# Kernel tuning notes

Hardware: AMD Instinct MI355X
Metric: run time of the kernel (lower is better)

## Reference

```python
import jax, jax.numpy as jnp
import numpy as np

H = 64
N_G, E_G = 30000, 60000
N_LG, E_LG = 60000, 60000


def setup_inputs() -> dict:
    key = jax.random.key(0)
    ks = jax.random.split(key, 30)
    rn = lambda k, s, sc=0.05: jax.random.normal(k, s, jnp.float32) * sc
    return {
        "gx": jax.random.normal(ks[0], (N_G, 20), jnp.float32),
        "g_edge_index": jax.random.randint(ks[1], (2, E_G), 0, N_G, jnp.int32),
        "g_edge_attr": jax.random.uniform(ks[2], (E_G, 4), dtype=jnp.float32),
        "lgx": jax.random.normal(ks[3], (N_LG, 5), jnp.float32),
        "lg_edge_index": jax.random.randint(ks[4], (2, E_LG), 0, N_LG, jnp.int32),
        "lg_edge_attr": jax.random.uniform(ks[5], (E_LG, 1), dtype=jnp.float32),
        "adduct": jax.random.normal(ks[6], (3,), jnp.float32),
        "lin0_w": rn(ks[7], (20, H)), "lin0_b": rn(ks[8], (H,)),
        "g_nn_w1": rn(ks[9], (4, H)), "g_nn_b1": rn(ks[10], (H,)),
        "g_nn_w2": rn(ks[11], (H, H * H), 0.01), "g_nn_b2": rn(ks[12], (H * H,), 0.01),
        "g_root": rn(ks[13], (H, H)), "g_bias": rn(ks[14], (H,)),
        "lin0_lg_w": rn(ks[15], (5, H)), "lin0_lg_b": rn(ks[16], (H,)),
        "lg_nn_w1": rn(ks[17], (1, H)), "lg_nn_b1": rn(ks[18], (H,)),
        "lg_nn_w2": rn(ks[19], (H, H * H), 0.01), "lg_nn_b2": rn(ks[20], (H * H,), 0.01),
        "lg_root": rn(ks[21], (H, H)), "lg_bias": rn(ks[22], (H,)),
        "bott_w": rn(ks[23], (H + H + 3, 384)), "bott_b": rn(ks[24], (384,)),
        "lin1_w": rn(ks[25], (384, 384)), "lin1_b": rn(ks[26], (384,)),
        "lin2_w": rn(ks[27], (384, 1)), "lin2_b": rn(ks[28], (1,)),
    }


def _ecc_branch(x_in, edge_index, edge_attr, w1, b1, w2, b2, root, bias, n_iters, num_nodes):
    """N iterations of NNConv(aggr='mean') + ReLU, then sum pool over nodes."""
    src, tgt = edge_index[0], edge_index[1]  # source->target flow (PyG default)
    # edge MLP -> per-edge [in, out] weight (edge_attr is loop-invariant, compute once)
    W = (jax.nn.relu(edge_attr @ w1 + b1) @ w2 + b2).reshape(-1, H, H)  # [E, H, H]
    cnt = jnp.maximum(
        jax.ops.segment_sum(jnp.ones((tgt.shape[0],), x_in.dtype), tgt, num_segments=num_nodes),
        1.0,
    )
    x = x_in
    for _ in range(n_iters):
        msg = jnp.einsum('ei,eio->eo', x[src], W)  # gather + batched matvec
        agg = jax.ops.segment_sum(msg, tgt, num_segments=num_nodes) / cnt[:, None]  # scatter-mean
        x = jax.nn.relu(x @ root + agg + bias)  # root transform + bias (NNConv defaults)
    return x.sum(axis=0)  # sum pooling -> [H]


def reference(gx, g_edge_index, g_edge_attr, lgx, lg_edge_index, lg_edge_attr, adduct,
              lin0_w, lin0_b, g_nn_w1, g_nn_b1, g_nn_w2, g_nn_b2, g_root, g_bias,
              lin0_lg_w, lin0_lg_b, lg_nn_w1, lg_nn_b1, lg_nn_w2, lg_nn_b2, lg_root, lg_bias,
              bott_w, bott_b, lin1_w, lin1_b, lin2_w, lin2_b):
    out_g = _ecc_branch(jax.nn.relu(gx @ lin0_w + lin0_b), g_edge_index, g_edge_attr,
                        g_nn_w1, g_nn_b1, g_nn_w2, g_nn_b2, g_root, g_bias, 3, N_G)
    out_lg = _ecc_branch(jax.nn.relu(lgx @ lin0_lg_w + lin0_lg_b), lg_edge_index, lg_edge_attr,
                         lg_nn_w1, lg_nn_b1, lg_nn_w2, lg_nn_b2, lg_root, lg_bias, 3, N_LG)
    out = jnp.concatenate([out_g, out_lg, adduct], axis=-1)  # [131]
    out = jax.nn.relu(out @ bott_w + bott_b)
    for _ in range(6):
        out = jax.nn.relu(out @ lin1_w + lin1_b)
    return out @ lin2_w + lin2_b  # [1]
```

## Files before the change

kernel.cpp:

```cpp
#include <hip/hip_runtime.h>

typedef unsigned short u16;
using short8_t  = __attribute__((ext_vector_type(8)))  short;
using float16_t = __attribute__((ext_vector_type(16))) float;
using float2v   = __attribute__((ext_vector_type(2)))  float;

#define NKT 260
#define DEG_CAP 32

__device__ __forceinline__ float bf2f(u16 b) { return __uint_as_float(((unsigned)b) << 16); }
__device__ __forceinline__ u16 f2bf(float f) {
  unsigned u = __float_as_uint(f);
  return (u16)((u + 0x7fffu + ((u >> 16) & 1u)) >> 16);
}

union U8 { short8_t s; uint4 v; unsigned u[4]; };

__device__ __forceinline__ short8_t scale8p(const float2v* xf2, float2v h2) {
  U8 out;
  #pragma unroll
  for (int p = 0; p < 4; ++p) {
    float2v r = xf2[p] * h2;
    out.u[p] = __builtin_amdgcn_perm(__float_as_uint(r[1]), __float_as_uint(r[0]), 0x07060302);
  }
  return out.s;
}

template<int IN>
__device__ __forceinline__ void affine_body(
    const float* __restrict__ Xin, const float* __restrict__ W, const float* __restrict__ Bv,
    u16* __restrict__ Xout, int N, int gid)
{
  int n = gid >> 6, o = gid & 63;
  if (n >= N) return;
  float acc = Bv[o];
  #pragma unroll
  for (int i = 0; i < IN; ++i)
    acc = fmaf(Xin[n * IN + i], W[i * 64 + o], acc);
  Xout[gid] = f2bf(fmaxf(acc, 0.f));
}

__global__ __launch_bounds__(256) void affine_all_kernel(
    const float* __restrict__ gx, const float* __restrict__ l0w, const float* __restrict__ l0b, u16* __restrict__ xg,
    const float* __restrict__ lgx, const float* __restrict__ llw, const float* __restrict__ llb, u16* __restrict__ xl,
    const float* __restrict__ gea, const float* __restrict__ gw1, const float* __restrict__ gb1, u16* __restrict__ hg,
    const float* __restrict__ lea, const float* __restrict__ lw1, const float* __restrict__ lb1, u16* __restrict__ hl,
    int B0, int B1, int B2, int NG, int NLG, int EG, int ELG)
{
  int b = blockIdx.x, t = threadIdx.x;
  if (b < B0)       affine_body<20>(gx, l0w, l0b, xg, NG, b * 256 + t);
  else if (b < B1)  affine_body<5>(lgx, llw, llb, xl, NLG, (b - B0) * 256 + t);
  else if (b < B2)  affine_body<4>(gea, gw1, gb1, hg, EG, (b - B1) * 256 + t);
  else              affine_body<1>(lea, lw1, lb1, hl, ELG, (b - B2) * 256 + t);
}

__device__ __forceinline__ void bpack_body(
    const float* __restrict__ w2, const float* __restrict__ b2, u16* __restrict__ Bp, int gid)
{
  if (gid >= NKT * 128) return;
  int lane = gid & 63;
  int nt = (gid >> 6) & 1;
  int kt = gid >> 7;
  int o = nt * 32 + (lane & 31);
  int kbase = kt * 16 + (lane >> 5) * 8;
  u16 vals[8];
  #pragma unroll
  for (int j = 0; j < 8; ++j) {
    int k = kbase + j;
    vals[j] = f2bf((k < 4096) ? w2[(k >> 6) * 4096 + (k & 63) * 64 + o]
                              : b2[(k - 4096) * 64 + o]);
  }
  uint4 pack;
  pack.x = (unsigned)vals[0] | ((unsigned)vals[1] << 16);
  pack.y = (unsigned)vals[2] | ((unsigned)vals[3] << 16);
  pack.z = (unsigned)vals[4] | ((unsigned)vals[5] << 16);
  pack.w = (unsigned)vals[6] | ((unsigned)vals[7] << 16);
  *(uint4*)(Bp + (size_t)gid * 8) = pack;
}

__device__ __forceinline__ void rootpack_body(const float* __restrict__ root, u16* __restrict__ Rp, int gid)
{
  if (gid >= 512) return;
  int lane = gid & 63;
  int nt = (gid >> 6) & 1;
  int kt = gid >> 7;
  int o = nt * 32 + (lane & 31);
  int kbase = kt * 16 + (lane >> 5) * 8;
  u16 vals[8];
  #pragma unroll
  for (int j = 0; j < 8; ++j) vals[j] = f2bf(root[(kbase + j) * 64 + o]);
  uint4 pack;
  pack.x = (unsigned)vals[0] | ((unsigned)vals[1] << 16);
  pack.y = (unsigned)vals[2] | ((unsigned)vals[3] << 16);
  pack.z = (unsigned)vals[4] | ((unsigned)vals[5] << 16);
  pack.w = (unsigned)vals[6] | ((unsigned)vals[7] << 16);
  *(uint4*)(Rp + (size_t)gid * 8) = pack;
}

__global__ __launch_bounds__(256) void pack_all_kernel(
    const float* __restrict__ gw2, const float* __restrict__ gb2, u16* __restrict__ bpg,
    const float* __restrict__ lw2, const float* __restrict__ lb2, u16* __restrict__ bpl,
    const float* __restrict__ groot, u16* __restrict__ rpg,
    const float* __restrict__ lroot, u16* __restrict__ rpl)
{
  int b = blockIdx.x, t = threadIdx.x;
  if (b < 130)       bpack_body(gw2, gb2, bpg, b * 256 + t);
  else if (b < 260)  bpack_body(lw2, lb2, bpl, (b - 130) * 256 + t);
  else if (b < 262)  rootpack_body(groot, rpg, (b - 260) * 256 + t);
  else               rootpack_body(lroot, rpl, (b - 262) * 256 + t);
}

__device__ __forceinline__ void hist_body(
    const int* __restrict__ eidx, int* __restrict__ cnt, int* __restrict__ elist, int E, int e)
{
  if (e < E) {
    int tg = eidx[E + e];
    int pos = atomicAdd(cnt + tg, 1);
    if (pos < DEG_CAP) elist[(size_t)tg * DEG_CAP + pos] = e;
  }
}

__global__ __launch_bounds__(256) void hist_kernel(
    const int* __restrict__ eig, int* __restrict__ cg, int* __restrict__ elg, int Eg, int nbg,
    const int* __restrict__ eil, int* __restrict__ cl, int* __restrict__ ell, int El)
{
  int b = blockIdx.x, t = threadIdx.x;
  if (b < nbg) hist_body(eig, cg, elg, Eg, b * 256 + t);
  else         hist_body(eil, cl, ell, El, (b - nbg) * 256 + t);
}

__global__ __launch_bounds__(256, 4) void msg_gemm_kernel(
    const u16* __restrict__ Xg, const u16* __restrict__ Hg, const u16* __restrict__ Bg,
    const int* __restrict__ eig, u16* __restrict__ Mg, int Eg, int nbg,
    const u16* __restrict__ Xl, const u16* __restrict__ Hl, const u16* __restrict__ Bl,
    const int* __restrict__ eil, u16* __restrict__ Ml, int El)
{
  __shared__ __align__(16) u16 sB[4][4096];

  const int b = blockIdx.x;
  const u16 *X, *Hh, *Bp; const int* eidx; u16* msg; int E, e0;
  if (b < nbg) { X = Xg; Hh = Hg; Bp = Bg; eidx = eig; msg = Mg; E = Eg; e0 = b * 128; }
  else         { X = Xl; Hh = Hl; Bp = Bl; eidx = eil; msg = Ml; E = El; e0 = (b - nbg) * 128; }

  const int t = threadIdx.x;
  const int lane = t & 63;
  const int wid = t >> 6;
  const int ml = lane & 31;
  const int q  = lane >> 5;

  #pragma unroll
  for (int c0 = 0; c0 < 3; ++c0) {
    const u16* src = Bp + (size_t)c0 * 4096 + (size_t)wid * 1024 + (size_t)lane * 8;
    u16* dst = &sB[c0][wid * 1024];
    __builtin_amdgcn_global_load_lds((const __attribute__((address_space(1))) void*)src,
                                     (__attribute__((address_space(3))) void*)dst, 16, 0, 0);
    __builtin_amdgcn_global_load_lds((const __attribute__((address_space(1))) void*)(src + 512),
                                     (__attribute__((address_space(3))) void*)(dst + 512), 16, 0, 0);
  }

  const int ea  = e0 + wid * 32 + ml;
  const int eac = ea < E ? ea : E - 1;
  const int sa  = eidx[eac];

  float2v xf2[4][4];
  {
    const u16* xp = X + (size_t)sa * 64 + q * 8;
    #pragma unroll
    for (int s = 0; s < 4; ++s) {
      U8 va;
      va.v = *(const uint4*)(xp + s * 16);
      #pragma unroll
      for (int p = 0; p < 4; ++p) {
        float2v r;
        r[0] = __uint_as_float(va.u[p] << 16);
        r[1] = __uint_as_float(va.u[p] & 0xffff0000u);
        xf2[s][p] = r;
      }
    }
  }

  const uint4* ha4 = (const uint4*)(Hh + (size_t)eac * 64);
  uint4 hcur = ha4[0], hnext = ha4[1];

  float16_t acc0, acc1;
  #pragma unroll
  for (int i = 0; i < 16; ++i) { acc0[i] = 0.f; acc1[i] = 0.f; }

  const u16* bsrc = Bp + (size_t)3 * 4096 + (size_t)wid * 1024 + (size_t)lane * 8;

  const short8_t* sb8 = (const short8_t*)&sB[0][0];

  asm volatile("s_waitcnt vmcnt(0)" ::: "memory");
  __builtin_amdgcn_sched_barrier(0);
  __builtin_amdgcn_s_barrier();

  for (int g = 0; g < 8; ++g) {
    float hsv[8];
    {
      const unsigned* hw = (const unsigned*)&hcur;
      #pragma unroll
      for (int w = 0; w < 4; ++w) {
        hsv[2 * w]     = __uint_as_float(hw[w] << 16);
        hsv[2 * w + 1] = __uint_as_float(hw[w] & 0xffff0000u);
      }
    }
    #pragma unroll
    for (int cc = 0; cc < 8; ++cc) {
      {
        __builtin_amdgcn_global_load_lds((const __attribute__((address_space(1))) void*)bsrc,
                                         (__attribute__((address_space(3))) void*)&sB[(cc + 3) & 3][wid * 1024], 16, 0, 0);
        __builtin_amdgcn_global_load_lds((const __attribute__((address_space(1))) void*)(bsrc + 512),
                                         (__attribute__((address_space(3))) void*)(&sB[(cc + 3) & 3][wid * 1024] + 512), 16, 0, 0);
        bsrc += 4096;
      }
      float2v h2; h2[0] = hsv[cc]; h2[1] = hsv[cc];
      const int sbase = (cc & 3) * 512;
      #pragma unroll
      for (int tt = 0; tt < 4; ++tt) {
        short8_t b0 = sb8[sbase + tt * 128 + lane];
        short8_t b1 = sb8[sbase + tt * 128 + 64 + lane];
        short8_t a0 = scale8p(xf2[tt], h2);
        acc0 = __builtin_amdgcn_mfma_f32_32x32x16_bf16(a0, b0, acc0, 0, 0, 0);
        acc1 = __builtin_amdgcn_mfma_f32_32x32x16_bf16(a0, b1, acc1, 0, 0, 0);
      }
      asm volatile("s_waitcnt lgkmcnt(0)" ::: "memory");
      asm volatile("s_waitcnt vmcnt(4)" ::: "memory");
      __builtin_amdgcn_sched_barrier(0);
      __builtin_amdgcn_s_barrier();
    }
    hcur = hnext;
    if (g < 6) hnext = ha4[g + 2];
  }

  {
    float2v h2; h2[0] = 1.0f; h2[1] = 1.0f;
    #pragma unroll
    for (int tt = 0; tt < 4; ++tt) {
      short8_t b0 = sb8[tt * 128 + lane];
      short8_t b1 = sb8[tt * 128 + 64 + lane];
      short8_t a0 = scale8p(xf2[tt], h2);
      acc0 = __builtin_amdgcn_mfma_f32_32x32x16_bf16(a0, b0, acc0, 0, 0, 0);
      acc1 = __builtin_amdgcn_mfma_f32_32x32x16_bf16(a0, b1, acc1, 0, 0, 0);
    }
  }

  #pragma unroll
  for (int reg = 0; reg < 16; ++reg) {
    int row = (reg & 3) + 8 * (reg >> 2) + 4 * q;
    int e1 = e0 + wid * 32 + row;
    if (e1 < E) {
      msg[(size_t)e1 * 64 + ml]      = f2bf(acc0[reg]);
      msg[(size_t)e1 * 64 + 32 + ml] = f2bf(acc1[reg]);
    }
  }
}

__global__ __launch_bounds__(256, 4) void update_kernel(
    const u16* __restrict__ Xig, const u16* __restrict__ Mgg, const int* __restrict__ cg,
    const int* __restrict__ elg, const u16* __restrict__ rpg, const float* __restrict__ bg,
    u16* __restrict__ Xog, int Ng, int nbg,
    const u16* __restrict__ Xil, const u16* __restrict__ Mgl, const int* __restrict__ cl,
    const int* __restrict__ ell, const u16* __restrict__ rpl, const float* __restrict__ bl,
    u16* __restrict__ Xol, int Nl)
{
  const int b = blockIdx.x;
  const u16 *Xin, *rootp, *msg; const float *bias; const int *cnt, *elist;
  u16* Xout; int N, n0;
  if (b < nbg) { Xin=Xig; msg=Mgg; cnt=cg; elist=elg; rootp=rpg; bias=bg; Xout=Xog; N=Ng; n0=b*128; }
  else         { Xin=Xil; msg=Mgl; cnt=cl; elist=ell; rootp=rpl; bias=bl; Xout=Xol; N=Nl; n0=(b-nbg)*128; }

  const int t = threadIdx.x;
  const int lane = t & 63;
  const int wid = t >> 6;
  const int ml = lane & 31;
  const int q  = lane >> 5;
  const int nbase = n0 + wid * 32;

  const int na = nbase + ml;
  const int nac = na < N ? na : N - 1;

  U8 xr[4];
  {
    const u16* xp = Xin + (size_t)nac * 64 + q * 8;
    #pragma unroll
    for (int s = 0; s < 4; ++s) xr[s].v = *(const uint4*)(xp + s * 16);
  }
  U8 rp[8];
  {
    const uint4* rpv = (const uint4*)rootp;
    #pragma unroll
    for (int i = 0; i < 8; ++i) rp[i].v = rpv[i * 64 + lane];
  }
  const float bias0 = bias[ml], bias1 = bias[32 + ml];

  float16_t acc0, acc1;
  #pragma unroll
  for (int i = 0; i < 16; ++i) { acc0[i] = 0.f; acc1[i] = 0.f; }
  #pragma unroll
  for (int kt = 0; kt < 4; ++kt) {
    acc0 = __builtin_amdgcn_mfma_f32_32x32x16_bf16(xr[kt].s, rp[kt * 2 + 0].s, acc0, 0, 0, 0);
    acc1 = __builtin_amdgcn_mfma_f32_32x32x16_bf16(xr[kt].s, rp[kt * 2 + 1].s, acc1, 0, 0, 0);
  }

  #pragma unroll
  for (int reg = 0; reg < 16; ++reg) {
    int row = (reg & 3) + 8 * (reg >> 2) + 4 * q;
    int nn = nbase + row;
    if (nn < N) {
      int c = cnt[nn];
      int cc = c < DEG_CAP ? c : DEG_CAP;
      const int* ep = elist + (size_t)nn * DEG_CAP;
      float a0 = 0.f, a1 = 0.f;
      int j = 0;
      for (; j + 4 <= cc; j += 4) {
        int e0i = ep[j], e1i = ep[j + 1], e2i = ep[j + 2], e3i = ep[j + 3];
        u16 m00 = msg[(size_t)e0i * 64 + ml], m01 = msg[(size_t)e0i * 64 + 32 + ml];
        u16 m10 = msg[(size_t)e1i * 64 + ml], m11 = msg[(size_t)e1i * 64 + 32 + ml];
        u16 m20 = msg[(size_t)e2i * 64 + ml], m21 = msg[(size_t)e2i * 64 + 32 + ml];
        u16 m30 = msg[(size_t)e3i * 64 + ml], m31 = msg[(size_t)e3i * 64 + 32 + ml];
        a0 += bf2f(m00) + bf2f(m10) + bf2f(m20) + bf2f(m30);
        a1 += bf2f(m01) + bf2f(m11) + bf2f(m21) + bf2f(m31);
      }
      for (; j < cc; ++j) {
        int e = ep[j];
        a0 += bf2f(msg[(size_t)e * 64 + ml]);
        a1 += bf2f(msg[(size_t)e * 64 + 32 + ml]);
      }
      float rc = (c > 1) ? (1.0f / (float)c) : 1.0f;
      float o0 = fmaxf(acc0[reg] + a0 * rc + bias0, 0.f);
      float o1 = fmaxf(acc1[reg] + a1 * rc + bias1, 0.f);
      Xout[(size_t)nn * 64 + ml]      = f2bf(o0);
      Xout[(size_t)nn * 64 + 32 + ml] = f2bf(o1);
    }
  }
}

__device__ __forceinline__ void pool_body(const u16* __restrict__ X, float* __restrict__ out64,
                                          int nchunks, int bid, int t)
{
  __shared__ float red[64];
  if (t < 64) red[t] = 0.f;
  __syncthreads();
  int gid = bid * 256 + t;
  float s[8];
  #pragma unroll
  for (int j = 0; j < 8; ++j) s[j] = 0.f;
  for (int i = gid; i < nchunks; i += 256 * 256) {
    uint4 v = ((const uint4*)X)[i];
    s[0] += bf2f((u16)(v.x & 0xffffu)); s[1] += bf2f((u16)(v.x >> 16));
    s[2] += bf2f((u16)(v.y & 0xffffu)); s[3] += bf2f((u16)(v.y >> 16));
    s[4] += bf2f((u16)(v.z & 0xffffu)); s[5] += bf2f((u16)(v.z >> 16));
    s[6] += bf2f((u16)(v.w & 0xffffu)); s[7] += bf2f((u16)(v.w >> 16));
  }
  int cg = (gid & 7) * 8;
  #pragma unroll
  for (int j = 0; j < 8; ++j) atomicAdd(red + cg + j, s[j]);
  __syncthreads();
  if (t < 64) atomicAdd(out64 + t, red[t]);
}

__global__ __launch_bounds__(256) void pool_kernel(
    const u16* __restrict__ Xg, float* __restrict__ og, int ncg,
    const u16* __restrict__ Xl, float* __restrict__ ol, int ncl)
{
  int b = blockIdx.x, t = threadIdx.x;
  if (b < 256) pool_body(Xg, og, ncg, b, t);
  else         pool_body(Xl, ol, ncl, b - 256, t);
}

__global__ __launch_bounds__(256) void prep_head_kernel(
    const float* __restrict__ pg, const float* __restrict__ plg, const float* __restrict__ adduct,
    float* __restrict__ v)
{
  int t = threadIdx.x;
  if (t < 131) v[t] = (t < 64) ? pg[t] : (t < 128 ? plg[t - 64] : adduct[t - 128]);
}

__global__ __launch_bounds__(256) void gemv_relu_kernel(
    const float* __restrict__ in, const float* __restrict__ W, const float* __restrict__ b,
    float* __restrict__ out, int Ni, int No)
{
  __shared__ float red[16][17];
  int t = threadIdx.x;
  int ol = t & 15, ig = t >> 4;
  int o = blockIdx.x * 16 + ol;
  float s = 0.f;
  for (int i = ig; i < Ni; i += 16)
    s = fmaf(in[i], W[i * No + o], s);
  red[ig][ol] = s;
  __syncthreads();
  if (t < 16) {
    int oo = blockIdx.x * 16 + t;
    float acc = b[oo];
    #pragma unroll
    for (int g = 0; g < 16; ++g) acc += red[g][t];
    out[oo] = fmaxf(acc, 0.f);
  }
}

__global__ __launch_bounds__(384) void final_kernel(
    const float* __restrict__ u, const float* __restrict__ l2w, const float* __restrict__ l2b,
    float* __restrict__ out)
{
  __shared__ float wred[6];
  int t = threadIdx.x;
  float p = u[t] * l2w[t];
  #pragma unroll
  for (int off = 32; off > 0; off >>= 1) p += __shfl_down(p, off);
  if ((t & 63) == 0) wred[t >> 6] = p;
  __syncthreads();
  if (t == 0) {
    float s = l2b[0];
    #pragma unroll
    for (int i = 0; i < 6; ++i) s += wred[i];
    out[0] = s;
  }
}

extern "C" void kernel_launch(void* const* d_in, const int* in_sizes, int n_in,
                              void* d_out, int out_size, void* d_ws, size_t ws_size,
                              hipStream_t stream)
{
  const int NG = 30000, EG = 60000, NLG = 60000, ELG = 60000;

  const float* gx      = (const float*)d_in[0];
  const int*   g_ei    = (const int*)  d_in[1];
  const float* g_ea    = (const float*)d_in[2];
  const float* lgx     = (const float*)d_in[3];
  const int*   lg_ei   = (const int*)  d_in[4];
  const float* lg_ea   = (const float*)d_in[5];
  const float* adduct  = (const float*)d_in[6];
  const float* lin0_w  = (const float*)d_in[7];
  const float* lin0_b  = (const float*)d_in[8];
  const float* g_w1    = (const float*)d_in[9];
  const float* g_b1    = (const float*)d_in[10];
  const float* g_w2    = (const float*)d_in[11];
  const float* g_b2    = (const float*)d_in[12];
  const float* g_root  = (const float*)d_in[13];
  const float* g_bias  = (const float*)d_in[14];
  const float* l0lg_w  = (const float*)d_in[15];
  const float* l0lg_b  = (const float*)d_in[16];
  const float* lg_w1   = (const float*)d_in[17];
  const float* lg_b1   = (const float*)d_in[18];
  const float* lg_w2   = (const float*)d_in[19];
  const float* lg_b2   = (const float*)d_in[20];
  const float* lg_root = (const float*)d_in[21];
  const float* lg_bias = (const float*)d_in[22];
  const float* bott_w  = (const float*)d_in[23];
  const float* bott_b  = (const float*)d_in[24];
  const float* lin1_w  = (const float*)d_in[25];
  const float* lin1_b  = (const float*)d_in[26];
  const float* lin2_w  = (const float*)d_in[27];
  const float* lin2_b  = (const float*)d_in[28];

  char* p = (char*)d_ws;
  auto alloc = [&](size_t bytes) { char* r = p; p += (bytes + 255) & ~(size_t)255; return r; };
  u16*   xg_a   = (u16*)  alloc((size_t)NG  * 64 * 2);
  u16*   xg_b   = (u16*)  alloc((size_t)NG  * 64 * 2);
  u16*   xl_a   = (u16*)  alloc((size_t)NLG * 64 * 2);
  u16*   xl_b   = (u16*)  alloc((size_t)NLG * 64 * 2);
  u16*   h_g    = (u16*)  alloc((size_t)EG  * 64 * 2);
  u16*   h_l    = (u16*)  alloc((size_t)ELG * 64 * 2);
  u16*   bp_g   = (u16*)  alloc((size_t)NKT * 128 * 8 * 2 + 16384);
  u16*   bp_l   = (u16*)  alloc((size_t)NKT * 128 * 8 * 2 + 16384);
  u16*   rp_g   = (u16*)  alloc(512 * 8 * 2);
  u16*   rp_l   = (u16*)  alloc(512 * 8 * 2);
  u16*   msg_g  = (u16*)  alloc((size_t)EG  * 64 * 2);
  u16*   msg_l  = (u16*)  alloc((size_t)ELG * 64 * 2);
  int*   cnt_g  = (int*)  alloc((size_t)NG  * 4);
  int*   cnt_l  = (int*)  alloc((size_t)NLG * 4);
  int*   el_g   = (int*)  alloc((size_t)NG  * DEG_CAP * 4);
  int*   el_l   = (int*)  alloc((size_t)NLG * DEG_CAP * 4);
  float* pool_g = (float*)alloc(64 * 4);
  float* pool_l = (float*)alloc(64 * 4);
  float* hv     = (float*)alloc(131 * 4);
  float* h0     = (float*)alloc(384 * 4);
  float* h1     = (float*)alloc(384 * 4);

  const int B0 = NG * 64 / 256, B1 = B0 + NLG * 64 / 256, B2 = B1 + EG * 64 / 256;
  const int Btot = B2 + ELG * 64 / 256;
  affine_all_kernel<<<Btot, 256, 0, stream>>>(
      gx, lin0_w, lin0_b, xg_a, lgx, l0lg_w, l0lg_b, xl_a,
      g_ea, g_w1, g_b1, h_g, lg_ea, lg_w1, lg_b1, h_l,
      B0, B1, B2, NG, NLG, EG, ELG);
  pack_all_kernel<<<264, 256, 0, stream>>>(g_w2, g_b2, bp_g, lg_w2, lg_b2, bp_l,
                                           g_root, rp_g, lg_root, rp_l);
  hipMemsetAsync(cnt_g, 0, (size_t)((char*)cnt_l - (char*)cnt_g) + (size_t)NLG * 4, stream);
  const int nhg = (EG + 255) / 256, nhl = (ELG + 255) / 256;
  hist_kernel<<<nhg + nhl, 256, 0, stream>>>(g_ei, cnt_g, el_g, EG, nhg, lg_ei, cnt_l, el_l, ELG);

  const int nbg_m = (EG + 127) / 128, nbl_m = (ELG + 127) / 128;
  const int nbg_u = (NG + 127) / 128, nbl_u = (NLG + 127) / 128;
  u16 *xgc = xg_a, *xgn = xg_b, *xlc = xl_a, *xln = xl_b;
  for (int it = 0; it < 3; ++it) {
    msg_gemm_kernel<<<nbg_m + nbl_m, 256, 0, stream>>>(
        xgc, h_g, bp_g, g_ei, msg_g, EG, nbg_m,
        xlc, h_l, bp_l, lg_ei, msg_l, ELG);
    update_kernel<<<nbg_u + nbl_u, 256, 0, stream>>>(
        xgc, msg_g, cnt_g, el_g, rp_g, g_bias, xgn, NG, nbg_u,
        xlc, msg_l, cnt_l, el_l, rp_l, lg_bias, xln, NLG);
    u16* tmp = xgc; xgc = xgn; xgn = tmp;
    tmp = xlc; xlc = xln; xln = tmp;
  }

  hipMemsetAsync(pool_g, 0, (size_t)((char*)pool_l - (char*)pool_g) + 64 * 4, stream);
  pool_kernel<<<512, 256, 0, stream>>>(xgc, pool_g, NG * 8, xlc, pool_l, NLG * 8);

  prep_head_kernel<<<1, 256, 0, stream>>>(pool_g, pool_l, adduct, hv);
  gemv_relu_kernel<<<24, 256, 0, stream>>>(hv, bott_w, bott_b, h0, 131, 384);
  float* ua = h0; float* ub = h1;
  for (int L = 0; L < 6; ++L) {
    gemv_relu_kernel<<<24, 256, 0, stream>>>(ua, lin1_w, lin1_b, ub, 384, 384);
    float* tmp = ua; ua = ub; ub = tmp;
  }
  final_kernel<<<1, 384, 0, stream>>>(ua, lin2_w, lin2_b, (float*)d_out);
}
```

Baseline: 512.6 us.

## Process two edge tiles per wave in msg GEMM to reuse streamed B

Each wave now handles 64 edges (two 32-row MFMA tiles) instead of 32, so every B tile streamed into shared memory feeds four MFMAs instead of two. This halves the number of blocks and the total global-to-LDS traffic for the large per-edge weight basis. To save registers, X is kept as packed bf16 and unpacked at each scale instead of being held as floats, and launch bounds are relaxed to 2 blocks per CU. The cost is lower occupancy and extra unpack ALU work per MFMA.

```diff
diff --git a/kernel.cpp b/kernel.cpp
--- a/kernel.cpp
+++ b/kernel.cpp
@@ -16,11 +16,14 @@
 
 union U8 { short8_t s; uint4 v; unsigned u[4]; };
 
-__device__ __forceinline__ short8_t scale8p(const float2v* xf2, float2v h2) {
+__device__ __forceinline__ short8_t scale8r(U8 xr, float2v h2) {
   U8 out;
   #pragma unroll
   for (int p = 0; p < 4; ++p) {
-    float2v r = xf2[p] * h2;
+    float2v r;
+    r[0] = __uint_as_float(xr.u[p] << 16);
+    r[1] = __uint_as_float(xr.u[p] & 0xffff0000u);
+    r = r * h2;
     out.u[p] = __builtin_amdgcn_perm(__float_as_uint(r[1]), __float_as_uint(r[0]), 0x07060302);
   }
   return out.s;
@@ -129,7 +132,7 @@
   else         hist_body(eil, cl, ell, El, (b - nbg) * 256 + t);
 }
 
-__global__ __launch_bounds__(256, 4) void msg_gemm_kernel(
+__global__ __launch_bounds__(256, 2) void msg_gemm_kernel(
     const u16* __restrict__ Xg, const u16* __restrict__ Hg, const u16* __restrict__ Bg,
     const int* __restrict__ eig, u16* __restrict__ Mg, int Eg, int nbg,
     const u16* __restrict__ Xl, const u16* __restrict__ Hl, const u16* __restrict__ Bl,
@@ -139,8 +142,8 @@
 
   const int b = blockIdx.x;
   const u16 *X, *Hh, *Bp; const int* eidx; u16* msg; int E, e0;
-  if (b < nbg) { X = Xg; Hh = Hg; Bp = Bg; eidx = eig; msg = Mg; E = Eg; e0 = b * 128; }
-  else         { X = Xl; Hh = Hl; Bp = Bl; eidx = eil; msg = Ml; E = El; e0 = (b - nbg) * 128; }
+  if (b < nbg) { X = Xg; Hh = Hg; Bp = Bg; eidx = eig; msg = Mg; E = Eg; e0 = b * 256; }
+  else         { X = Xl; Hh = Hl; Bp = Bl; eidx = eil; msg = Ml; E = El; e0 = (b - nbg) * 256; }
 
   const int t = threadIdx.x;
   const int lane = t & 63;
@@ -158,33 +161,31 @@
                                      (__attribute__((address_space(3))) void*)(dst + 512), 16, 0, 0);
   }
 
-  const int ea  = e0 + wid * 32 + ml;
+  const int ea  = e0 + wid * 64 + ml;
+  const int eb  = ea + 32;
   const int eac = ea < E ? ea : E - 1;
-  const int sa  = eidx[eac];
-
-  float2v xf2[4][4];
+  const int ebc = eb < E ? eb : E - 1;
+  const int sa  = eidx[eac], sb = eidx[ebc];
+
+  U8 xra[4], xrb[4];
   {
-    const u16* xp = X + (size_t)sa * 64 + q * 8;
+    const u16* xpa = X + (size_t)sa * 64 + q * 8;
+    const u16* xpb = X + (size_t)sb * 64 + q * 8;
     #pragma unroll
     for (int s = 0; s < 4; ++s) {
-      U8 va;
-      va.v = *(const uint4*)(xp + s * 16);
-      #pragma unroll
-      for (int p = 0; p < 4; ++p) {
-        float2v r;
-        r[0] = __uint_as_float(va.u[p] << 16);
-        r[1] = __uint_as_float(va.u[p] & 0xffff0000u);
-        xf2[s][p] = r;
-      }
+      xra[s].v = *(const uint4*)(xpa + s * 16);
+      xrb[s].v = *(const uint4*)(xpb + s * 16);
     }
   }
 
   const uint4* ha4 = (const uint4*)(Hh + (size_t)eac * 64);
-  uint4 hcur = ha4[0], hnext = ha4[1];
-
-  float16_t acc0, acc1;
-  #pragma unroll
-  for (int i = 0; i < 16; ++i) { acc0[i] = 0.f; acc1[i] = 0.f; }
+  const uint4* hb4 = (const uint4*)(Hh + (size_t)ebc * 64);
+  uint4 hc0 = ha4[0], hn0 = ha4[1];
+  uint4 hc1 = hb4[0], hn1 = hb4[1];
+
+  float16_t acc00, acc01, acc10, acc11;
+  #pragma unroll
+  for (int i = 0; i < 16; ++i) { acc00[i] = 0.f; acc01[i] = 0.f; acc10[i] = 0.f; acc11[i] = 0.f; }
 
   const u16* bsrc = Bp + (size_t)3 * 4096 + (size_t)wid * 1024 + (size_t)lane * 8;
 
@@ -195,15 +196,6 @@
   __builtin_amdgcn_s_barrier();
 
   for (int g = 0; g < 8; ++g) {
-    float hsv[8];
-    {
-      const unsigned* hw = (const unsigned*)&hcur;
-      #pragma unroll
-      for (int w = 0; w < 4; ++w) {
-        hsv[2 * w]     = __uint_as_float(hw[w] << 16);
-        hsv[2 * w + 1] = __uint_as_float(hw[w] & 0xffff0000u);
-      }
-    }
     #pragma unroll
     for (int cc = 0; cc < 8; ++cc) {
       {
@@ -213,23 +205,30 @@
                                          (__attribute__((address_space(3))) void*)(&sB[(cc + 3) & 3][wid * 1024] + 512), 16, 0, 0);
         bsrc += 4096;
       }
-      float2v h2; h2[0] = hsv[cc]; h2[1] = hsv[cc];
+      unsigned w0 = ((const unsigned*)&hc0)[cc >> 1];
+      unsigned w1 = ((const unsigned*)&hc1)[cc >> 1];
+      float2v h20, h21;
+      h20[0] = h20[1] = bf2f((u16)((cc & 1) ? (w0 >> 16) : (w0 & 0xffffu)));
+      h21[0] = h21[1] = bf2f((u16)((cc & 1) ? (w1 >> 16) : (w1 & 0xffffu)));
       const int sbase = (cc & 3) * 512;
       #pragma unroll
       for (int tt = 0; tt < 4; ++tt) {
         short8_t b0 = sb8[sbase + tt * 128 + lane];
         short8_t b1 = sb8[sbase + tt * 128 + 64 + lane];
-        short8_t a0 = scale8p(xf2[tt], h2);
-        acc0 = __builtin_amdgcn_mfma_f32_32x32x16_bf16(a0, b0, acc0, 0, 0, 0);
-        acc1 = __builtin_amdgcn_mfma_f32_32x32x16_bf16(a0, b1, acc1, 0, 0, 0);
+        short8_t a0 = scale8r(xra[tt], h20);
+        short8_t a1 = scale8r(xrb[tt], h21);
+        acc00 = __builtin_amdgcn_mfma_f32_32x32x16_bf16(a0, b0, acc00, 0, 0, 0);
+        acc01 = __builtin_amdgcn_mfma_f32_32x32x16_bf16(a0, b1, acc01, 0, 0, 0);
+        acc10 = __builtin_amdgcn_mfma_f32_32x32x16_bf16(a1, b0, acc10, 0, 0, 0);
+        acc11 = __builtin_amdgcn_mfma_f32_32x32x16_bf16(a1, b1, acc11, 0, 0, 0);
       }
       asm volatile("s_waitcnt lgkmcnt(0)" ::: "memory");
       asm volatile("s_waitcnt vmcnt(4)" ::: "memory");
       __builtin_amdgcn_sched_barrier(0);
       __builtin_amdgcn_s_barrier();
     }
-    hcur = hnext;
-    if (g < 6) hnext = ha4[g + 2];
+    hc0 = hn0; hc1 = hn1;
+    if (g < 6) { hn0 = ha4[g + 2]; hn1 = hb4[g + 2]; }
   }
 
   {
@@ -238,19 +237,27 @@
     for (int tt = 0; tt < 4; ++tt) {
       short8_t b0 = sb8[tt * 128 + lane];
       short8_t b1 = sb8[tt * 128 + 64 + lane];
-      short8_t a0 = scale8p(xf2[tt], h2);
-      acc0 = __builtin_amdgcn_mfma_f32_32x32x16_bf16(a0, b0, acc0, 0, 0, 0);
-      acc1 = __builtin_amdgcn_mfma_f32_32x32x16_bf16(a0, b1, acc1, 0, 0, 0);
+      short8_t a0 = scale8r(xra[tt], h2);
+      short8_t a1 = scale8r(xrb[tt], h2);
+      acc00 = __builtin_amdgcn_mfma_f32_32x32x16_bf16(a0, b0, acc00, 0, 0, 0);
+      acc01 = __builtin_amdgcn_mfma_f32_32x32x16_bf16(a0, b1, acc01, 0, 0, 0);
+      acc10 = __builtin_amdgcn_mfma_f32_32x32x16_bf16(a1, b0, acc10, 0, 0, 0);
+      acc11 = __builtin_amdgcn_mfma_f32_32x32x16_bf16(a1, b1, acc11, 0, 0, 0);
     }
   }
 
   #pragma unroll
   for (int reg = 0; reg < 16; ++reg) {
     int row = (reg & 3) + 8 * (reg >> 2) + 4 * q;
-    int e1 = e0 + wid * 32 + row;
+    int e1 = e0 + wid * 64 + row;
+    int e2 = e1 + 32;
     if (e1 < E) {
-      msg[(size_t)e1 * 64 + ml]      = f2bf(acc0[reg]);
-      msg[(size_t)e1 * 64 + 32 + ml] = f2bf(acc1[reg]);
+      msg[(size_t)e1 * 64 + ml]      = f2bf(acc00[reg]);
+      msg[(size_t)e1 * 64 + 32 + ml] = f2bf(acc01[reg]);
+    }
+    if (e2 < E) {
+      msg[(size_t)e2 * 64 + ml]      = f2bf(acc10[reg]);
+      msg[(size_t)e2 * 64 + 32 + ml] = f2bf(acc11[reg]);
     }
   }
 }
@@ -489,7 +496,7 @@
   const int nhg = (EG + 255) / 256, nhl = (ELG + 255) / 256;
   hist_kernel<<<nhg + nhl, 256, 0, stream>>>(g_ei, cnt_g, el_g, EG, nhg, lg_ei, cnt_l, el_l, ELG);
 
-  const int nbg_m = (EG + 127) / 128, nbl_m = (ELG + 127) / 128;
+  const int nbg_m = (EG + 255) / 256, nbl_m = (ELG + 255) / 256;
   const int nbg_u = (NG + 127) / 128, nbl_u = (NLG + 127) / 128;
   u16 *xgc = xg_a, *xgn = xg_b, *xlc = xl_a, *xln = xl_b;
   for (int it = 0; it < 3; ++it) {
```

After: 491.7 us. -4.1%, faster.
